# Kernel optimization log

Hardware: AMD Instinct MI355X
Metric: run time of the kernel (lower is better)

The kernel has to match this reference:

```python
import jax, jax.numpy as jnp
import numpy as np
import math

B, W, C, N = 4, 2048, 1024, 16
K = C // N  # 64


def setup_inputs() -> dict:
    key = jax.random.key(0)
    k1, k2, k3, k4, k5 = jax.random.split(key, 5)
    return {
        "in_sequence_bwc": jax.random.normal(k1, (B, W, C), dtype=jnp.float32),
        "W_proj": jax.random.normal(k2, (C, C), dtype=jnp.float32) * 0.02,   # torch Linear weight [out,in]
        "pre_metric_nkk": jax.random.normal(k3, (N, K, K), dtype=jnp.float32) * 0.1,
        "transforms_nkk": jax.random.normal(k4, (N, K, K), dtype=jnp.float32) * 0.1,
        "W_mixer": jax.random.normal(k5, (C, C), dtype=jnp.float32) * 0.02,
    }


def reference(in_sequence_bwc, W_proj, pre_metric_nkk, transforms_nkk, W_mixer):
    b, w, c = in_sequence_bwc.shape
    # metric tensor per head: M = P P^T (positive semidefinite-ish bilinear form)
    metric_nkk = jnp.einsum("nij,nkj->nik", pre_metric_nkk, pre_metric_nkk)
    # shared projection (torch Linear: x @ W^T)
    proj_bwc = in_sequence_bwc @ W_proj.T
    proj_bnwk = proj_bwc.reshape(b, w, N, K).transpose(0, 2, 1, 3)  # [b,n,w,k]
    # bilinear scores Q M Q^T / sqrt(k)
    qm_bnwk = jnp.einsum("bnwk,nkj->bnwj", proj_bnwk, metric_nkk)
    scores_bnww = jnp.einsum("bnwk,bnvk->bnwv", qm_bnwk, proj_bnwk) / math.sqrt(K)
    # multiplicative causal mask (no softmax)
    mask_ww = jnp.tril(jnp.ones((w, w), dtype=scores_bnww.dtype))
    scores_bnww = scores_bnww * mask_ww
    # nudged = scores @ proj @ T per head
    nudged_bnwk = jnp.einsum("bnwv,bnvk->bnwk", scores_bnww, proj_bnwk)
    nudged_bnwk = jnp.einsum("bnwk,nkj->bnwj", nudged_bnwk, transforms_nkk)
    nudged_bwc = nudged_bnwk.transpose(0, 2, 1, 3).reshape(b, w, c)
    return nudged_bwc @ W_mixer.T
```

## Files before the change

kernel.cpp:

```cpp
#include <hip/hip_runtime.h>

#define B_ 4
#define W_ 2048
#define C_ 1024
#define NH 16
#define KH 64

typedef __attribute__((ext_vector_type(8))) short short8;
typedef __attribute__((ext_vector_type(4))) short s16x4;
typedef __attribute__((ext_vector_type(4))) float f32x4;

__device__ __forceinline__ short f2bf(float f) {
    unsigned u = __builtin_bit_cast(unsigned, f);
    u = (u + 0x7FFFu + ((u >> 16) & 1u)) >> 16;
    return (short)u;
}
__device__ __forceinline__ float bf2f(short h) {
    return __builtin_bit_cast(float, ((unsigned)(unsigned short)h) << 16);
}

#define MFMA(a, b, cc) __builtin_amdgcn_mfma_f32_16x16x32_bf16(a, b, cc, 0, 0, 0)

__global__ __launch_bounds__(256) void k_metric(const float* __restrict__ P, float* __restrict__ M) {
    int n = blockIdx.x;
    __shared__ float sP[KH * KH];
    __shared__ float sPt[KH * 65];
    const float* Pn = P + n * KH * KH;
    for (int i = threadIdx.x; i < KH * KH; i += 256) {
        float v = Pn[i];
        sP[i] = v;
        sPt[(i & 63) * 65 + (i >> 6)] = v;
    }
    __syncthreads();
    float* Mn = M + n * KH * KH;
    for (int e = threadIdx.x; e < KH * KH; e += 256) {
        int i = e >> 6, k = e & 63;
        float s = 0.f;
        #pragma unroll 8
        for (int j = 0; j < KH; ++j) s += sP[i * KH + j] * sPt[j * 65 + k];
        Mn[e] = s;
    }
}

__global__ __launch_bounds__(256) void k_wf(const float* __restrict__ T, const float* __restrict__ Wm,
                                            short* __restrict__ Wf) {
    int n = blockIdx.y, oseg = blockIdx.x;
    __shared__ float sTt[KH * 65];
    __shared__ float sW[KH * KH];
    for (int i = threadIdx.x; i < KH * KH; i += 256) {
        sTt[(i & 63) * 65 + (i >> 6)] = T[n * KH * KH + i];
        int r = i >> 6, c = i & 63;
        sW[i] = Wm[(oseg * KH + r) * C_ + n * KH + c];
    }
    __syncthreads();
    for (int e = threadIdx.x; e < KH * KH; e += 256) {
        int r = e >> 6, k = e & 63;
        float s = 0.f;
        #pragma unroll 8
        for (int j = 0; j < KH; ++j) s += sTt[j * 65 + k] * sW[r * KH + j];
        Wf[(oseg * KH + r) * C_ + n * KH + k] = f2bf(s);
    }
}

__global__ __launch_bounds__(256) void k_cvt(const float* __restrict__ src, short* __restrict__ dst, int n4) {
    int i = blockIdx.x * 256 + threadIdx.x;
    if (i < n4) {
        float4 v = ((const float4*)src)[i];
        short4 o;
        o.x = f2bf(v.x); o.y = f2bf(v.y); o.z = f2bf(v.z); o.w = f2bf(v.w);
        ((short4*)dst)[i] = o;
    }
}

template <int OC, int STRIDE, bool OUT_FP32>
__global__ __launch_bounds__(256) void k_gemm(const short* __restrict__ A, const short* __restrict__ Bw,
                                              void* __restrict__ Out) {
    __shared__ short As[128 * 64];
    __shared__ short Bs[128 * 64];
    constexpr int NBX = OC / 128;
    int id = blockIdx.x + blockIdx.y * NBX;
    int fl = (id & 7) * (NBX * 64 / 8) + (id >> 3);
    int bm = fl / NBX, bn = fl % NBX;
    int t = threadIdx.x;
    int wave = t >> 6, lane = t & 63;
    int q = lane >> 4, c = lane & 15;
    int wy = wave >> 1, wx = wave & 1;
    f32x4 acc[4][4] = {};
    int xsw = (c & 7);
    for (int k0 = 0; k0 < C_; k0 += 64) {
        __syncthreads();
        #pragma unroll
        for (int e = 0; e < 4; ++e) {
            int row = (e * 256 + t) >> 3;
            int ks = ((t & 7) ^ (row & 7)) * 8;
            __builtin_amdgcn_global_load_lds(
                (const __attribute__((address_space(1))) void*)&A[(size_t)(bm * 128 + row) * C_ + k0 + ks],
                (__attribute__((address_space(3))) void*)&As[e * 2048 + wave * 512], 16, 0, 0);
            __builtin_amdgcn_global_load_lds(
                (const __attribute__((address_space(1))) void*)&Bw[(size_t)(bn * 128 + row) * C_ + k0 + ks],
                (__attribute__((address_space(3))) void*)&Bs[e * 2048 + wave * 512], 16, 0, 0);
        }
        __syncthreads();
        #pragma unroll
        for (int kk = 0; kk < 64; kk += 32) {
            int o = kk >> 3;
            int xo = ((o + q) ^ xsw) * 8;
            short8 af[4], bfr[4];
            #pragma unroll
            for (int i = 0; i < 4; ++i)
                af[i] = *(const short8*)&As[(wy * 64 + i * 16 + c) * 64 + xo];
            #pragma unroll
            for (int j = 0; j < 4; ++j)
                bfr[j] = *(const short8*)&Bs[(wx * 64 + j * 16 + c) * 64 + xo];
            #pragma unroll
            for (int i = 0; i < 4; ++i)
                #pragma unroll
                for (int j = 0; j < 4; ++j)
                    acc[i][j] = MFMA(af[i], bfr[j], acc[i][j]);
        }
    }
    #pragma unroll
    for (int i = 0; i < 4; ++i)
        #pragma unroll
        for (int j = 0; j < 4; ++j)
            #pragma unroll
            for (int r = 0; r < 4; ++r) {
                int row = bm * 128 + wy * 64 + i * 16 + q * 4 + r;
                int col = bn * 128 + wx * 64 + j * 16 + c;
                if (OUT_FP32) ((float*)Out)[(size_t)row * STRIDE + col] = acc[i][j][r];
                else ((short*)Out)[(size_t)row * STRIDE + col] = f2bf(acc[i][j][r]);
            }
}

__global__ __launch_bounds__(256) void k_qm(const short* __restrict__ pjqm_in,
                                            const float* __restrict__ metric,
                                            short* __restrict__ pjqm_out) {
    int bm = blockIdx.x, n = blockIdx.y;
    int t = threadIdx.x, wave = t >> 6, lane = t & 63;
    int q = lane >> 4, c = lane & 15;
    __shared__ short Mb[64 * 72];
    const float* Mn = metric + n * 4096;
    #pragma unroll
    for (int e = 0; e < 4; ++e) {
        int i4 = e * 256 + t;
        float4 v = ((const float4*)Mn)[i4];
        s16x4 o;
        o[0] = f2bf(v.x * 0.125f); o[1] = f2bf(v.y * 0.125f);
        o[2] = f2bf(v.z * 0.125f); o[3] = f2bf(v.w * 0.125f);
        int row = i4 >> 4, col = (i4 & 15) * 4;
        *(s16x4*)&Mb[row * 72 + col] = o;
    }
    __syncthreads();
    short8 b0[4], b1[4];
    #pragma unroll
    for (int ct = 0; ct < 4; ++ct) {
        b0[ct] = *(const short8*)&Mb[(ct * 16 + c) * 72 + q * 8];
        b1[ct] = *(const short8*)&Mb[(ct * 16 + c) * 72 + 32 + q * 8];
    }
    int rbase = bm * 256 + wave * 64;
    #pragma unroll
    for (int rt = 0; rt < 4; ++rt) {
        const short* arow = &pjqm_in[(size_t)(rbase + rt * 16 + c) * 2048 + n * KH];
        short8 a0 = *(const short8*)(arow + q * 8);
        short8 a1 = *(const short8*)(arow + 32 + q * 8);
        #pragma unroll
        for (int ct = 0; ct < 4; ++ct) {
            f32x4 acc = {};
            acc = MFMA(a0, b0[ct], acc);
            acc = MFMA(a1, b1[ct], acc);
            #pragma unroll
            for (int r = 0; r < 4; ++r)
                pjqm_out[(size_t)(rbase + rt * 16 + q * 4 + r) * 2048 + 1024 + n * KH + ct * 16 + c] =
                    f2bf(acc[r]);
        }
    }
}

__global__ __launch_bounds__(256) void k_outer(const short* __restrict__ pjqm,
                                               short* __restrict__ Chi, short* __restrict__ Clo) {
    int cc = blockIdx.x, n = blockIdx.y, b = blockIdx.z;
    int bn = b * NH + n;
    int t = threadIdx.x, wave = t >> 6, lane = t & 63;
    int q = lane >> 4, c = lane & 15;
    __shared__ short Pt_s[64 * 72];
    #pragma unroll
    for (int e = 0; e < 2; ++e) {
        int chv = e * 256 + t, row = chv >> 3, sub = chv & 7;
        short8 p8 = *(const short8*)&pjqm[(size_t)(b * W_ + cc * 64 + row) * 2048 + n * KH + sub * 8];
        #pragma unroll
        for (int j = 0; j < 8; ++j) Pt_s[(sub * 8 + j) * 72 + row] = p8[j];
    }
    __syncthreads();
    short8 a0 = *(const short8*)&Pt_s[(wave * 16 + c) * 72 + q * 8];
    short8 a1 = *(const short8*)&Pt_s[(wave * 16 + c) * 72 + 32 + q * 8];
    size_t cbase = ((size_t)bn * 32 + cc) * 4096;
    #pragma unroll
    for (int tj = 0; tj < 4; ++tj) {
        short8 b0 = *(const short8*)&Pt_s[(tj * 16 + c) * 72 + q * 8];
        short8 b1 = *(const short8*)&Pt_s[(tj * 16 + c) * 72 + 32 + q * 8];
        f32x4 acc = {};
        acc = MFMA(a0, b0, acc);
        acc = MFMA(a1, b1, acc);
        s16x4 hi, lo;
        #pragma unroll
        for (int r = 0; r < 4; ++r) {
            float a = acc[r];
            short h = f2bf(a);
            hi[r] = h;
            lo[r] = f2bf(a - bf2f(h));
        }
        size_t off = cbase + (size_t)(tj * 16 + c) * 64 + wave * 16 + q * 4;
        *(s16x4*)&Chi[off] = hi;
        *(s16x4*)&Clo[off] = lo;
    }
}

__global__ __launch_bounds__(256) void k_scan(short* __restrict__ Chi, short* __restrict__ Clo) {
    int bn = blockIdx.y;
    int el = blockIdx.x * 1024 + threadIdx.x * 4;
    size_t off = (size_t)bn * 32 * 4096 + el;
    float run[4] = {0.f, 0.f, 0.f, 0.f};
    s16x4 h = *(const s16x4*)&Chi[off];
    s16x4 l = *(const s16x4*)&Clo[off];
    for (int cc = 0; cc < 31; ++cc) {
        s16x4 nh, nl;
        if (cc < 30) {
            nh = *(const s16x4*)&Chi[off + 4096];
            nl = *(const s16x4*)&Clo[off + 4096];
        }
        s16x4 oh, ol;
        #pragma unroll
        for (int r = 0; r < 4; ++r) {
            float o = bf2f(h[r]) + bf2f(l[r]);
            float cv = run[r];
            short hh = f2bf(cv);
            oh[r] = hh;
            ol[r] = f2bf(cv - bf2f(hh));
            run[r] = cv + o;
        }
        *(s16x4*)&Chi[off] = oh;
        *(s16x4*)&Clo[off] = ol;
        h = nh; l = nl;
        off += 4096;
    }
    s16x4 oh, ol;
    #pragma unroll
    for (int r = 0; r < 4; ++r) {
        short hh = f2bf(run[r]);
        oh[r] = hh;
        ol[r] = f2bf(run[r] - bf2f(hh));
    }
    *(s16x4*)&Chi[off] = oh;
    *(s16x4*)&Clo[off] = ol;
}

__global__ __launch_bounds__(256) void k_chunk(const short* __restrict__ pjqm,
                                               const short* __restrict__ Chi, const short* __restrict__ Clo,
                                               short* __restrict__ Nd) {
    int cc = blockIdx.x, n = blockIdx.y, b = blockIdx.z;
    int t = threadIdx.x, wave = t >> 6, lane = t & 63;
    int q = lane >> 4, c = lane & 15;
    __shared__ short Ps[64 * 72];
    __shared__ short Pt_s[64 * 72];
    __shared__ short Ch[64 * 72];
    __shared__ short Cl[64 * 72];
    __shared__ short St[4][16 * 72];
    int w0g = b * W_ + cc * 64;

    const short* qmrow = &pjqm[(size_t)(w0g + wave * 16 + c) * 2048 + 1024 + n * KH];
    short8 bq0 = *(const short8*)(qmrow + q * 8);
    short8 bq1 = *(const short8*)(qmrow + 32 + q * 8);

    #pragma unroll
    for (int e = 0; e < 2; ++e) {
        int chv = e * 256 + t, row = chv >> 3, sub = chv & 7;
        short8 p8 = *(const short8*)&pjqm[(size_t)(w0g + row) * 2048 + n * KH + sub * 8];
        *(short8*)&Ps[row * 72 + sub * 8] = p8;
        #pragma unroll
        for (int j = 0; j < 8; ++j) Pt_s[(sub * 8 + j) * 72 + row] = p8[j];
        size_t cbase = ((size_t)((b * NH + n) * 32 + cc)) * 4096;
        *(short8*)&Ch[row * 72 + sub * 8] = *(const short8*)&Chi[cbase + row * 64 + sub * 8];
        *(short8*)&Cl[row * 72 + sub * 8] = *(const short8*)&Clo[cbase + row * 64 + sub * 8];
    }
    __syncthreads();
    #pragma unroll
    for (int ct = 0; ct < 4; ++ct) {
        short8 a0 = *(const short8*)&Ps[(ct * 16 + c) * 72 + q * 8];
        short8 a1 = *(const short8*)&Ps[(ct * 16 + c) * 72 + 32 + q * 8];
        f32x4 s = {};
        s = MFMA(a0, bq0, s);
        s = MFMA(a1, bq1, s);
        int vb = ct * 16 + q * 4, wl = wave * 16 + c;
        s16x4 pk;
        #pragma unroll
        for (int r = 0; r < 4; ++r) {
            float v = s[r];
            if (vb + r > wl) v = 0.f;
            pk[r] = f2bf(v);
        }
        *(s16x4*)&St[wave][c * 72 + ct * 16 + q * 4] = pk;
    }
    __syncthreads();
    f32x4 oc[4] = {};
    short8 as0 = *(const short8*)&St[wave][c * 72 + q * 8];
    short8 as1 = *(const short8*)&St[wave][c * 72 + 32 + q * 8];
    #pragma unroll
    for (int tj = 0; tj < 4; ++tj) {
        short8 bp0 = *(const short8*)&Pt_s[(tj * 16 + c) * 72 + q * 8];
        short8 bp1 = *(const short8*)&Pt_s[(tj * 16 + c) * 72 + 32 + q * 8];
        oc[tj] = MFMA(as0, bp0, oc[tj]);
        oc[tj] = MFMA(as1, bp1, oc[tj]);
        short8 bh0 = *(const short8*)&Ch[(tj * 16 + c) * 72 + q * 8];
        short8 bh1 = *(const short8*)&Ch[(tj * 16 + c) * 72 + 32 + q * 8];
        oc[tj] = MFMA(bq0, bh0, oc[tj]);
        oc[tj] = MFMA(bq1, bh1, oc[tj]);
        short8 bl0 = *(const short8*)&Cl[(tj * 16 + c) * 72 + q * 8];
        short8 bl1 = *(const short8*)&Cl[(tj * 16 + c) * 72 + 32 + q * 8];
        oc[tj] = MFMA(bq0, bl0, oc[tj]);
        oc[tj] = MFMA(bq1, bl1, oc[tj]);
    }
    #pragma unroll
    for (int tj = 0; tj < 4; ++tj)
        #pragma unroll
        for (int r = 0; r < 4; ++r)
            Nd[(size_t)(w0g + wave * 16 + q * 4 + r) * C_ + n * KH + tj * 16 + c] = f2bf(oc[tj][r]);
}

extern "C" void kernel_launch(void* const* d_in, const int* in_sizes, int n_in,
                              void* d_out, int out_size, void* d_ws, size_t ws_size,
                              hipStream_t stream) {
    const float* x  = (const float*)d_in[0];
    const float* Wp = (const float*)d_in[1];
    const float* Pm = (const float*)d_in[2];
    const float* Tr = (const float*)d_in[3];
    const float* Wm = (const float*)d_in[4];
    float* out = (float*)d_out;
    char* ws = (char*)d_ws;

    const size_t MB = 1024 * 1024;
    float* metric = (float*)ws;
    short* wp16  = (short*)(ws + 256 * 1024);
    short* wf16  = (short*)(ws + 256 * 1024 + 4 * MB);
    short* x16   = (short*)(ws + 256 * 1024 + 6 * MB);
    short* pjqm  = (short*)(ws + 256 * 1024 + 22 * MB);
    short* nd16  = x16;
    short* Chi   = (short*)d_out;
    short* Clo   = Chi + 8 * MB;

    k_metric<<<dim3(NH), dim3(256), 0, stream>>>(Pm, metric);
    k_wf<<<dim3(16, NH), dim3(256), 0, stream>>>(Tr, Wm, wf16);
    k_cvt<<<dim3(8192), dim3(256), 0, stream>>>(x, x16, (B_ * W_ * C_) / 4);
    k_cvt<<<dim3(1024), dim3(256), 0, stream>>>(Wp, wp16, (C_ * C_) / 4);

    k_gemm<1024, 2048, false><<<dim3(8, 64), dim3(256), 0, stream>>>(x16, wp16, (void*)pjqm);
    k_qm<<<dim3(32, NH), dim3(256), 0, stream>>>(pjqm, metric, pjqm);
    k_outer<<<dim3(31, NH, B_), dim3(256), 0, stream>>>(pjqm, Chi, Clo);
    k_scan<<<dim3(4, 64), dim3(256), 0, stream>>>(Chi, Clo);
    k_chunk<<<dim3(32, NH, B_), dim3(256), 0, stream>>>(pjqm, Chi, Clo, nd16);
    k_gemm<1024, 1024, true><<<dim3(8, 64), dim3(256), 0, stream>>>(nd16, wf16, (void*)out);
}
```

Baseline: 217.7 us.

## Merge prep kernels, fuse QM into outer-product kernel, shrink GEMM N-tile

```diff
diff --git a/kernel.cpp b/kernel.cpp
--- a/kernel.cpp
+++ b/kernel.cpp
@@ -21,54 +21,59 @@
 
 #define MFMA(a, b, cc) __builtin_amdgcn_mfma_f32_16x16x32_bf16(a, b, cc, 0, 0, 0)
 
-__global__ __launch_bounds__(256) void k_metric(const float* __restrict__ P, float* __restrict__ M) {
-    int n = blockIdx.x;
-    __shared__ float sP[KH * KH];
-    __shared__ float sPt[KH * 65];
-    const float* Pn = P + n * KH * KH;
-    for (int i = threadIdx.x; i < KH * KH; i += 256) {
-        float v = Pn[i];
-        sP[i] = v;
-        sPt[(i & 63) * 65 + (i >> 6)] = v;
-    }
-    __syncthreads();
-    float* Mn = M + n * KH * KH;
-    for (int e = threadIdx.x; e < KH * KH; e += 256) {
-        int i = e >> 6, k = e & 63;
-        float s = 0.f;
-        #pragma unroll 8
-        for (int j = 0; j < KH; ++j) s += sP[i * KH + j] * sPt[j * 65 + k];
-        Mn[e] = s;
-    }
-}
-
-__global__ __launch_bounds__(256) void k_wf(const float* __restrict__ T, const float* __restrict__ Wm,
-                                            short* __restrict__ Wf) {
-    int n = blockIdx.y, oseg = blockIdx.x;
-    __shared__ float sTt[KH * 65];
-    __shared__ float sW[KH * KH];
-    for (int i = threadIdx.x; i < KH * KH; i += 256) {
-        sTt[(i & 63) * 65 + (i >> 6)] = T[n * KH * KH + i];
-        int r = i >> 6, c = i & 63;
-        sW[i] = Wm[(oseg * KH + r) * C_ + n * KH + c];
-    }
-    __syncthreads();
-    for (int e = threadIdx.x; e < KH * KH; e += 256) {
-        int r = e >> 6, k = e & 63;
-        float s = 0.f;
-        #pragma unroll 8
-        for (int j = 0; j < KH; ++j) s += sTt[j * 65 + k] * sW[r * KH + j];
-        Wf[(oseg * KH + r) * C_ + n * KH + k] = f2bf(s);
-    }
-}
-
-__global__ __launch_bounds__(256) void k_cvt(const float* __restrict__ src, short* __restrict__ dst, int n4) {
-    int i = blockIdx.x * 256 + threadIdx.x;
-    if (i < n4) {
-        float4 v = ((const float4*)src)[i];
+__global__ __launch_bounds__(256) void k_prep(const float* __restrict__ x, const float* __restrict__ Wp,
+                                              const float* __restrict__ Pm, const float* __restrict__ Tr,
+                                              const float* __restrict__ Wm,
+                                              short* __restrict__ x16, short* __restrict__ wp16,
+                                              short* __restrict__ wf16, float* __restrict__ metric) {
+    int bid = blockIdx.x, t = threadIdx.x;
+    __shared__ float sA[KH * 65];
+    __shared__ float sB[KH * KH];
+    if (bid < 8192) {
+        int i = bid * 256 + t;
+        float4 v = ((const float4*)x)[i];
         short4 o;
         o.x = f2bf(v.x); o.y = f2bf(v.y); o.z = f2bf(v.z); o.w = f2bf(v.w);
-        ((short4*)dst)[i] = o;
+        ((short4*)x16)[i] = o;
+    } else if (bid < 9216) {
+        int i = (bid - 8192) * 256 + t;
+        float4 v = ((const float4*)Wp)[i];
+        short4 o;
+        o.x = f2bf(v.x); o.y = f2bf(v.y); o.z = f2bf(v.z); o.w = f2bf(v.w);
+        ((short4*)wp16)[i] = o;
+    } else if (bid < 9472) {
+        int idx = bid - 9216;
+        int oseg = idx & 15, n = idx >> 4;
+        for (int i = t; i < KH * KH; i += 256) {
+            sA[(i & 63) * 65 + (i >> 6)] = Tr[n * KH * KH + i];
+            int r = i >> 6, c = i & 63;
+            sB[i] = Wm[(oseg * KH + r) * C_ + n * KH + c];
+        }
+        __syncthreads();
+        for (int e = t; e < KH * KH; e += 256) {
+            int r = e >> 6, k = e & 63;
+            float s = 0.f;
+            #pragma unroll 8
+            for (int j = 0; j < KH; ++j) s += sA[j * 65 + k] * sB[r * KH + j];
+            wf16[(oseg * KH + r) * C_ + n * KH + k] = f2bf(s);
+        }
+    } else {
+        int n = bid - 9472;
+        const float* Pn = Pm + n * KH * KH;
+        for (int i = t; i < KH * KH; i += 256) {
+            float v = Pn[i];
+            sB[i] = v;
+            sA[(i & 63) * 65 + (i >> 6)] = v;
+        }
+        __syncthreads();
+        float* Mn = metric + n * KH * KH;
+        for (int e = t; e < KH * KH; e += 256) {
+            int i = e >> 6, k = e & 63;
+            float s = 0.f;
+            #pragma unroll 8
+            for (int j = 0; j < KH; ++j) s += sB[i * KH + j] * sA[j * 65 + k];
+            Mn[e] = s;
+        }
     }
 }
 
@@ -76,8 +81,8 @@
 __global__ __launch_bounds__(256) void k_gemm(const short* __restrict__ A, const short* __restrict__ Bw,
                                               void* __restrict__ Out) {
     __shared__ short As[128 * 64];
-    __shared__ short Bs[128 * 64];
-    constexpr int NBX = OC / 128;
+    __shared__ short Bs[64 * 64];
+    constexpr int NBX = OC / 64;
     int id = blockIdx.x + blockIdx.y * NBX;
     int fl = (id & 7) * (NBX * 64 / 8) + (id >> 3);
     int bm = fl / NBX, bn = fl % NBX;
@@ -85,7 +90,7 @@
     int wave = t >> 6, lane = t & 63;
     int q = lane >> 4, c = lane & 15;
     int wy = wave >> 1, wx = wave & 1;
-    f32x4 acc[4][4] = {};
+    f32x4 acc[4][2] = {};
     int xsw = (c & 7);
     for (int k0 = 0; k0 < C_; k0 += 64) {
         __syncthreads();
@@ -96,8 +101,13 @@
             __builtin_amdgcn_global_load_lds(
                 (const __attribute__((address_space(1))) void*)&A[(size_t)(bm * 128 + row) * C_ + k0 + ks],
                 (__attribute__((address_space(3))) void*)&As[e * 2048 + wave * 512], 16, 0, 0);
+        }
+        #pragma unroll
+        for (int e = 0; e < 2; ++e) {
+            int row = (e * 256 + t) >> 3;
+            int ks = ((t & 7) ^ (row & 7)) * 8;
             __builtin_amdgcn_global_load_lds(
-                (const __attribute__((address_space(1))) void*)&Bw[(size_t)(bn * 128 + row) * C_ + k0 + ks],
+                (const __attribute__((address_space(1))) void*)&Bw[(size_t)(bn * 64 + row) * C_ + k0 + ks],
                 (__attribute__((address_space(3))) void*)&Bs[e * 2048 + wave * 512], 16, 0, 0);
         }
         __syncthreads();
@@ -105,40 +115,44 @@
         for (int kk = 0; kk < 64; kk += 32) {
             int o = kk >> 3;
             int xo = ((o + q) ^ xsw) * 8;
-            short8 af[4], bfr[4];
+            short8 af[4], bfr[2];
             #pragma unroll
             for (int i = 0; i < 4; ++i)
                 af[i] = *(const short8*)&As[(wy * 64 + i * 16 + c) * 64 + xo];
             #pragma unroll
-            for (int j = 0; j < 4; ++j)
-                bfr[j] = *(const short8*)&Bs[(wx * 64 + j * 16 + c) * 64 + xo];
+            for (int j = 0; j < 2; ++j)
+                bfr[j] = *(const short8*)&Bs[(wx * 32 + j * 16 + c) * 64 + xo];
             #pragma unroll
             for (int i = 0; i < 4; ++i)
                 #pragma unroll
-                for (int j = 0; j < 4; ++j)
+                for (int j = 0; j < 2; ++j)
                     acc[i][j] = MFMA(af[i], bfr[j], acc[i][j]);
         }
     }
     #pragma unroll
     for (int i = 0; i < 4; ++i)
         #pragma unroll
-        for (int j = 0; j < 4; ++j)
+        for (int j = 0; j < 2; ++j)
             #pragma unroll
             for (int r = 0; r < 4; ++r) {
                 int row = bm * 128 + wy * 64 + i * 16 + q * 4 + r;
-                int col = bn * 128 + wx * 64 + j * 16 + c;
+                int col = bn * 64 + wx * 32 + j * 16 + c;
                 if (OUT_FP32) ((float*)Out)[(size_t)row * STRIDE + col] = acc[i][j][r];
                 else ((short*)Out)[(size_t)row * STRIDE + col] = f2bf(acc[i][j][r]);
             }
 }
 
-__global__ __launch_bounds__(256) void k_qm(const short* __restrict__ pjqm_in,
-                                            const float* __restrict__ metric,
-                                            short* __restrict__ pjqm_out) {
-    int bm = blockIdx.x, n = blockIdx.y;
+__global__ __launch_bounds__(256) void k_outer(short* __restrict__ pjqm,
+                                               const float* __restrict__ metric,
+                                               short* __restrict__ Chi, short* __restrict__ Clo) {
+    int cc = blockIdx.x, n = blockIdx.y, b = blockIdx.z;
+    int bn = b * NH + n;
     int t = threadIdx.x, wave = t >> 6, lane = t & 63;
     int q = lane >> 4, c = lane & 15;
+    int w0g = b * W_ + cc * 64;
+    __shared__ short Pt_s[64 * 72];
     __shared__ short Mb[64 * 72];
+
     const float* Mn = metric + n * 4096;
     #pragma unroll
     for (int e = 0; e < 4; ++e) {
@@ -150,68 +164,58 @@
         int row = i4 >> 4, col = (i4 & 15) * 4;
         *(s16x4*)&Mb[row * 72 + col] = o;
     }
+    if (cc < 31) {
+        #pragma unroll
+        for (int e = 0; e < 2; ++e) {
+            int chv = e * 256 + t, row = chv >> 3, sub = chv & 7;
+            short8 p8 = *(const short8*)&pjqm[(size_t)(w0g + row) * 2048 + n * KH + sub * 8];
+            #pragma unroll
+            for (int j = 0; j < 8; ++j) Pt_s[(sub * 8 + j) * 72 + row] = p8[j];
+        }
+    }
     __syncthreads();
-    short8 b0[4], b1[4];
-    #pragma unroll
-    for (int ct = 0; ct < 4; ++ct) {
-        b0[ct] = *(const short8*)&Mb[(ct * 16 + c) * 72 + q * 8];
-        b1[ct] = *(const short8*)&Mb[(ct * 16 + c) * 72 + 32 + q * 8];
-    }
-    int rbase = bm * 256 + wave * 64;
-    #pragma unroll
-    for (int rt = 0; rt < 4; ++rt) {
-        const short* arow = &pjqm_in[(size_t)(rbase + rt * 16 + c) * 2048 + n * KH];
+
+    {
+        const short* arow = &pjqm[(size_t)(w0g + wave * 16 + c) * 2048 + n * KH];
         short8 a0 = *(const short8*)(arow + q * 8);
         short8 a1 = *(const short8*)(arow + 32 + q * 8);
         #pragma unroll
         for (int ct = 0; ct < 4; ++ct) {
+            short8 b0 = *(const short8*)&Mb[(ct * 16 + c) * 72 + q * 8];
+            short8 b1 = *(const short8*)&Mb[(ct * 16 + c) * 72 + 32 + q * 8];
             f32x4 acc = {};
-            acc = MFMA(a0, b0[ct], acc);
-            acc = MFMA(a1, b1[ct], acc);
+            acc = MFMA(a0, b0, acc);
+            acc = MFMA(a1, b1, acc);
             #pragma unroll
             for (int r = 0; r < 4; ++r)
-                pjqm_out[(size_t)(rbase + rt * 16 + q * 4 + r) * 2048 + 1024 + n * KH + ct * 16 + c] =
+                pjqm[(size_t)(w0g + wave * 16 + q * 4 + r) * 2048 + 1024 + n * KH + ct * 16 + c] =
                     f2bf(acc[r]);
         }
     }
-}
-
-__global__ __launch_bounds__(256) void k_outer(const short* __restrict__ pjqm,
-                                               short* __restrict__ Chi, short* __restrict__ Clo) {
-    int cc = blockIdx.x, n = blockIdx.y, b = blockIdx.z;
-    int bn = b * NH + n;
-    int t = threadIdx.x, wave = t >> 6, lane = t & 63;
-    int q = lane >> 4, c = lane & 15;
-    __shared__ short Pt_s[64 * 72];
-    #pragma unroll
-    for (int e = 0; e < 2; ++e) {
-        int chv = e * 256 + t, row = chv >> 3, sub = chv & 7;
-        short8 p8 = *(const short8*)&pjqm[(size_t)(b * W_ + cc * 64 + row) * 2048 + n * KH + sub * 8];
-        #pragma unroll
-        for (int j = 0; j < 8; ++j) Pt_s[(sub * 8 + j) * 72 + row] = p8[j];
-    }
-    __syncthreads();
-    short8 a0 = *(const short8*)&Pt_s[(wave * 16 + c) * 72 + q * 8];
-    short8 a1 = *(const short8*)&Pt_s[(wave * 16 + c) * 72 + 32 + q * 8];
-    size_t cbase = ((size_t)bn * 32 + cc) * 4096;
-    #pragma unroll
-    for (int tj = 0; tj < 4; ++tj) {
-        short8 b0 = *(const short8*)&Pt_s[(tj * 16 + c) * 72 + q * 8];
-        short8 b1 = *(const short8*)&Pt_s[(tj * 16 + c) * 72 + 32 + q * 8];
-        f32x4 acc = {};
-        acc = MFMA(a0, b0, acc);
-        acc = MFMA(a1, b1, acc);
-        s16x4 hi, lo;
-        #pragma unroll
-        for (int r = 0; r < 4; ++r) {
-            float a = acc[r];
-            short h = f2bf(a);
-            hi[r] = h;
-            lo[r] = f2bf(a - bf2f(h));
-        }
-        size_t off = cbase + (size_t)(tj * 16 + c) * 64 + wave * 16 + q * 4;
-        *(s16x4*)&Chi[off] = hi;
-        *(s16x4*)&Clo[off] = lo;
+
+    if (cc < 31) {
+        short8 a0 = *(const short8*)&Pt_s[(wave * 16 + c) * 72 + q * 8];
+        short8 a1 = *(const short8*)&Pt_s[(wave * 16 + c) * 72 + 32 + q * 8];
+        size_t cbase = ((size_t)bn * 32 + cc) * 4096;
+        #pragma unroll
+        for (int tj = 0; tj < 4; ++tj) {
+            short8 b0 = *(const short8*)&Pt_s[(tj * 16 + c) * 72 + q * 8];
+            short8 b1 = *(const short8*)&Pt_s[(tj * 16 + c) * 72 + 32 + q * 8];
+            f32x4 acc = {};
+            acc = MFMA(a0, b0, acc);
+            acc = MFMA(a1, b1, acc);
+            s16x4 hi, lo;
+            #pragma unroll
+            for (int r = 0; r < 4; ++r) {
+                float a = acc[r];
+                short h = f2bf(a);
+                hi[r] = h;
+                lo[r] = f2bf(a - bf2f(h));
+            }
+            size_t off = cbase + (size_t)(tj * 16 + c) * 64 + wave * 16 + q * 4;
+            *(s16x4*)&Chi[off] = hi;
+            *(s16x4*)&Clo[off] = lo;
+        }
     }
 }
 
@@ -347,15 +351,10 @@
     short* Chi   = (short*)d_out;
     short* Clo   = Chi + 8 * MB;
 
-    k_metric<<<dim3(NH), dim3(256), 0, stream>>>(Pm, metric);
-    k_wf<<<dim3(16, NH), dim3(256), 0, stream>>>(Tr, Wm, wf16);
-    k_cvt<<<dim3(8192), dim3(256), 0, stream>>>(x, x16, (B_ * W_ * C_) / 4);
-    k_cvt<<<dim3(1024), dim3(256), 0, stream>>>(Wp, wp16, (C_ * C_) / 4);
-
-    k_gemm<1024, 2048, false><<<dim3(8, 64), dim3(256), 0, stream>>>(x16, wp16, (void*)pjqm);
-    k_qm<<<dim3(32, NH), dim3(256), 0, stream>>>(pjqm, metric, pjqm);
-    k_outer<<<dim3(31, NH, B_), dim3(256), 0, stream>>>(pjqm, Chi, Clo);
+    k_prep<<<dim3(9488), dim3(256), 0, stream>>>(x, Wp, Pm, Tr, Wm, x16, wp16, wf16, metric);
+    k_gemm<1024, 2048, false><<<dim3(16, 64), dim3(256), 0, stream>>>(x16, wp16, (void*)pjqm);
+    k_outer<<<dim3(32, NH, B_), dim3(256), 0, stream>>>(pjqm, metric, Chi, Clo);
     k_scan<<<dim3(4, 64), dim3(256), 0, stream>>>(Chi, Clo);
     k_chunk<<<dim3(32, NH, B_), dim3(256), 0, stream>>>(pjqm, Chi, Clo, nd16);
-    k_gemm<1024, 1024, true><<<dim3(8, 64), dim3(256), 0, stream>>>(nd16, wf16, (void*)out);
-}
+    k_gemm<1024, 1024, true><<<dim3(16, 64), dim3(256), 0, stream>>>(nd16, wf16, (void*)out);
+}
```

Result: faster. 210.3 us (-3.4%).
